# Optimization experiments

Hardware: AMD Instinct MI355X
Metric: run time of the kernel (lower is better)

Reference implementation:

```python
import jax, jax.numpy as jnp
import numpy as np

D_MODEL = 1024
N_HEAD = 16
HEAD_DIM = D_MODEL // N_HEAD


def setup_inputs() -> dict:
    key = jax.random.key(0)
    ks = jax.random.split(key, 11)
    B, L = 1, 2048
    s = 1.0 / np.sqrt(D_MODEL)
    return {
        "q": jax.random.normal(ks[0], (B, L, D_MODEL), jnp.float32),
        "k": jax.random.normal(ks[1], (B, L, D_MODEL), jnp.float32),
        "v": jax.random.normal(ks[2], (B, L, D_MODEL), jnp.float32),
        "w_q": jax.random.normal(ks[3], (D_MODEL, D_MODEL), jnp.float32) * s,
        "b_q": jax.random.normal(ks[4], (D_MODEL,), jnp.float32) * s,
        "w_k": jax.random.normal(ks[5], (D_MODEL, D_MODEL), jnp.float32) * s,
        "b_k": jax.random.normal(ks[6], (D_MODEL,), jnp.float32) * s,
        "w_v": jax.random.normal(ks[7], (D_MODEL, D_MODEL), jnp.float32) * s,
        "b_v": jax.random.normal(ks[8], (D_MODEL,), jnp.float32) * s,
        "w_o": jax.random.normal(ks[9], (D_MODEL, D_MODEL), jnp.float32) * s,
        "b_o": jax.random.normal(ks[10], (D_MODEL,), jnp.float32) * s,
    }


def _split_heads(x):
    # [B, L, D] -> [B, H, L, Dh]
    B, L, D = x.shape
    return x.reshape(B, L, N_HEAD, HEAD_DIM).transpose(0, 2, 1, 3)


def reference(q, k, v, w_q, b_q, w_k, b_k, w_v, b_v, w_o, b_o):
    # Linear projections (torch Linear: x @ W.T + b; here weights stored as [D_in, D_out])
    qh = _split_heads(q @ w_q + b_q)
    kh = _split_heads(k @ w_k + b_k)
    vh = _split_heads(v @ w_v + b_v)
    scale = 1.0 / jnp.sqrt(jnp.asarray(HEAD_DIM, qh.dtype))
    # [B, H, Lq, Lk] full score matrix (faithful to naive implementation)
    score = jnp.einsum("bhqd,bhkd->bhqk", qh, kh) * scale
    attn = jax.nn.softmax(score, axis=-1)
    out = jnp.einsum("bhqk,bhkd->bhqd", attn, vh)
    # concat heads: [B, H, L, Dh] -> [B, L, D]
    B, H, L, Dh = out.shape
    out = out.transpose(0, 2, 1, 3).reshape(B, L, H * Dh)
    return out @ w_o + b_o  # dropout p=0.0 -> identity
```

## Files before the change

kernel.cpp:

```cpp
#include <hip/hip_runtime.h>
#include <hip/hip_bf16.h>
#include <stdint.h>
#include <stddef.h>

typedef __bf16 bf16_t;
typedef __bf16 v8bf __attribute__((ext_vector_type(8)));
typedef __bf16 v4bf __attribute__((ext_vector_type(4)));
typedef float  v4f  __attribute__((ext_vector_type(4)));

#define L_SEQ 2048
#define DM    1024
#define NH    16
#define LOG2E 1.44269504088896340736f
#define SCL   (0.125f * LOG2E)

__device__ __forceinline__ void async_cp16(const void* g, void* l) {
  __builtin_amdgcn_global_load_lds(
      (__attribute__((address_space(1))) void*)(g),
      (__attribute__((address_space(3))) void*)(l),
      16, 0, 0);
}

__device__ __forceinline__ v4f mfma16(v8bf a, v8bf b, v4f c) {
  return __builtin_amdgcn_mfma_f32_16x16x32_bf16(a, b, c, 0, 0, 0);
}

#if __has_builtin(__builtin_amdgcn_exp2f)
__device__ __forceinline__ float fast_exp2(float x) { return __builtin_amdgcn_exp2f(x); }
#else
__device__ __forceinline__ float fast_exp2(float x) { return exp2f(x); }
#endif

__global__ void k_prep(
    const float* __restrict__ q, const float* __restrict__ k,
    const float* __restrict__ v,
    const float* __restrict__ w0, const float* __restrict__ w1,
    const float* __restrict__ w2, const float* __restrict__ w3,
    bf16_t* __restrict__ Qb, bf16_t* __restrict__ Kb, bf16_t* __restrict__ Vb,
    bf16_t* __restrict__ o0, bf16_t* __restrict__ o1,
    bf16_t* __restrict__ o2, bf16_t* __restrict__ o3)
{
  const int z = blockIdx.z;
  const int tid = threadIdx.x;
  if (z < 4) {
    const float* in = (z == 0) ? w0 : (z == 1) ? w1 : (z == 2) ? w2 : w3;
    bf16_t*     out = (z == 0) ? o0 : (z == 1) ? o1 : (z == 2) ? o2 : o3;
    __shared__ float t[64 * 65];
    const int r0 = blockIdx.y * 64, c0 = blockIdx.x * 64;
#pragma unroll
    for (int p = 0; p < 16; ++p) {
      const int idx = p * 256 + tid;
      const int r = idx >> 6, c = idx & 63;
      t[r * 65 + c] = in[(size_t)(r0 + r) * DM + c0 + c];
    }
    __syncthreads();
#pragma unroll
    for (int p = 0; p < 16; ++p) {
      const int idx = p * 256 + tid;
      const int c = idx >> 6, r = idx & 63;
      out[(size_t)(c0 + c) * DM + r0 + r] = (bf16_t)t[r * 65 + c];
    }
  } else {
    const float* src = (z == 4) ? q : (z == 5) ? k : v;
    bf16_t*      dst = (z == 4) ? Qb : (z == 5) ? Kb : Vb;
    const int n4 = (L_SEQ * DM) / 4;
    const int base = (blockIdx.y * 16 + blockIdx.x) * 256 + tid;
#pragma unroll
    for (int i = base; i < n4; i += 16 * 16 * 256) {
      v4f x = ((const v4f*)src)[i];
      v4bf y;
      y[0] = (bf16_t)x[0]; y[1] = (bf16_t)x[1];
      y[2] = (bf16_t)x[2]; y[3] = (bf16_t)x[3];
      ((v4bf*)dst)[i] = y;
    }
  }
}

template <typename OutT>
__device__ __forceinline__ void gemm128x64_body(
    const bf16_t* __restrict__ A, const bf16_t* __restrict__ Bt,
    const float* __restrict__ biasN, const float* __restrict__ biasM,
    OutT* __restrict__ C, int M, int N, int K, int bx, int by)
{
  __shared__ __align__(16) bf16_t As[2][128 * 64];
  __shared__ __align__(16) bf16_t Bs[2][64 * 64];
  const int tid  = threadIdx.x;
  const int w    = tid >> 6;
  const int lane = tid & 63;
  const int l16  = lane & 15;
  const int q4   = lane >> 4;
  const int m0   = by * 128, n0 = bx * 64;
  const int wm   = (w >> 1) * 64, wn = (w & 1) * 32;
  const int lr = lane >> 3, lc = lane & 7;

  v4f acc[4][2];
#pragma unroll
  for (int i = 0; i < 4; ++i)
#pragma unroll
    for (int j = 0; j < 2; ++j) {
      v4f z = {0.f, 0.f, 0.f, 0.f};
      acc[i][j] = z;
    }

  auto stage = [&](int k0, int buf) {
#pragma unroll
    for (int c = 0; c < 4; ++c) {
      const int row = 32 * w + 8 * c + lr;
      const int q   = lc ^ (row & 7);
      async_cp16(A + (size_t)(m0 + row) * K + k0 + q * 8,
                 &As[buf][(32 * w + 8 * c) * 64]);
    }
#pragma unroll
    for (int c = 0; c < 2; ++c) {
      const int row = 16 * w + 8 * c + lr;
      const int q   = lc ^ (row & 7);
      async_cp16(Bt + (size_t)(n0 + row) * K + k0 + q * 8,
                 &Bs[buf][(16 * w + 8 * c) * 64]);
    }
  };

  stage(0, 0);
  __syncthreads();

  const int nk = K >> 6;
  for (int kt = 0; kt < nk; ++kt) {
    if (kt + 1 < nk) stage((kt + 1) << 6, (kt + 1) & 1);
    const int buf = kt & 1;
#pragma unroll
    for (int ks = 0; ks < 2; ++ks) {
      v8bf af[4], bf_[2];
#pragma unroll
      for (int mi = 0; mi < 4; ++mi) {
        const int row = wm + mi * 16 + l16;
        const int pc  = (4 * ks + q4) ^ (row & 7);
        af[mi] = *(const v8bf*)(&As[buf][row * 64 + pc * 8]);
      }
#pragma unroll
      for (int ni = 0; ni < 2; ++ni) {
        const int row = wn + ni * 16 + l16;
        const int pc  = (4 * ks + q4) ^ (row & 7);
        bf_[ni] = *(const v8bf*)(&Bs[buf][row * 64 + pc * 8]);
      }
#pragma unroll
      for (int mi = 0; mi < 4; ++mi)
#pragma unroll
        for (int ni = 0; ni < 2; ++ni)
          acc[mi][ni] = mfma16(af[mi], bf_[ni], acc[mi][ni]);
    }
    __syncthreads();
  }

  float bvn[2] = {0.f, 0.f};
  if (biasN) {
#pragma unroll
    for (int ni = 0; ni < 2; ++ni) bvn[ni] = biasN[n0 + wn + ni * 16 + l16];
  }
#pragma unroll
  for (int mi = 0; mi < 4; ++mi) {
#pragma unroll
    for (int r = 0; r < 4; ++r) {
      const int row = m0 + wm + mi * 16 + q4 * 4 + r;
      const float bm = biasM ? biasM[row] : 0.f;
#pragma unroll
      for (int ni = 0; ni < 2; ++ni) {
        const int col = n0 + wn + ni * 16 + l16;
        C[(size_t)row * N + col] = (OutT)(acc[mi][ni][r] + bvn[ni] + bm);
      }
    }
  }
}

__global__ __launch_bounds__(256, 3) void k_gemm_fused(
    const bf16_t* __restrict__ Qb, const bf16_t* __restrict__ Kb,
    const bf16_t* __restrict__ Vb,
    const bf16_t* __restrict__ Wqkt,
    const bf16_t* __restrict__ Wvt,
    const float* __restrict__ bq, const float* __restrict__ bk,
    const float* __restrict__ bv,
    bf16_t* __restrict__ QKo, bf16_t* __restrict__ Vtr)
{
  const int idx = blockIdx.x;
  const bf16_t *A, *Bt;
  const float *bN = nullptr, *bM = nullptr;
  bf16_t* C;
  int M, N, bx, by;
  if (idx < 512) {
    by = idx & 15; bx = idx >> 4;
    A  = (bx < 16) ? Qb : Kb;
    Bt = Wqkt;
    bN = (bx < 16) ? bq : (bk - DM);
    C  = QKo; M = L_SEQ; N = 2 * DM;
  } else {
    const int i2 = idx - 512;
    by = i2 & 7; bx = i2 >> 3;
    A  = Wvt; Bt = Vb; bM = bv;
    C  = Vtr; M = DM; N = L_SEQ;
  }
  gemm128x64_body<bf16_t>(A, Bt, bN, bM, C, M, N, DM, bx, by);
}

__global__ __launch_bounds__(256, 3) void k_gemm_oproj(
    const bf16_t* __restrict__ A, const bf16_t* __restrict__ Bt,
    const float* __restrict__ bias, float* __restrict__ C)
{
  gemm128x64_body<float>(A, Bt, bias, nullptr, C, L_SEQ, DM, DM,
                         blockIdx.x, blockIdx.y);
}

__global__ __launch_bounds__(256, 2) void k_attn(
    const bf16_t* __restrict__ QKp,
    const bf16_t* __restrict__ Vt,
    bf16_t* __restrict__ AO)
{
  constexpr int LD = 2 * DM;
  const int lid = blockIdx.x;
  const int hd  = (lid & 7) + 8 * ((lid >> 3) & 1);
  const int q0  = (lid >> 4) * 64;
  const int tid = threadIdx.x, w = tid >> 6, lane = tid & 63;
  const int l16 = lane & 15, q4 = lane >> 4;
  const int lr8 = lane >> 3, lc8 = lane & 7;

  __shared__ __align__(16) bf16_t Ks[2][64 * 64];
  __shared__ __align__(16) bf16_t Vs[2][64 * 64];
  __shared__ __align__(16) bf16_t QPs[64 * 72];

  const bf16_t* Qp = QKp;
  const bf16_t* Kp = QKp + DM;

  const bf16_t* pK[2];
  const bf16_t* pV[2];
#pragma unroll
  for (int c = 0; c < 2; ++c) {
    const int row = 16 * w + 8 * c + lr8;
    const int q   = lc8 ^ (row & 7);
    pK[c] = Kp + (size_t)row * LD + hd * 64 + q * 8;
    pV[c] = Vt + (size_t)(hd * 64 + row) * L_SEQ + q * 8;
  }
  auto stage_kv = [&](int j0, int buf) {
#pragma unroll
    for (int c = 0; c < 2; ++c) {
      async_cp16(pK[c] + (size_t)j0 * LD, &Ks[buf][(16 * w + 8 * c) * 64]);
      async_cp16(pV[c] + j0,              &Vs[buf][(16 * w + 8 * c) * 64]);
    }
  };

#pragma unroll
  for (int c = 0; c < 2; ++c) {
    const int row = 16 * w + 8 * c + lr8;
    const int q   = lc8 ^ (row & 7);
    async_cp16(Qp + (size_t)(q0 + row) * LD + hd * 64 + q * 8,
               &QPs[(16 * w + 8 * c) * 64]);
  }
  stage_kv(0, 0);
  __syncthreads();

  const int prow = 16 * w + l16;
  v8bf bq[2];
#pragma unroll
  for (int ks = 0; ks < 2; ++ks) {
    const int pc = (4 * ks + q4) ^ (prow & 7);
    bq[ks] = *(const v8bf*)(&QPs[prow * 64 + pc * 8]);
  }
  __syncthreads();

  float l_run = 0.f;
  v4f od[4];
#pragma unroll
  for (int d = 0; d < 4; ++d) { v4f z = {0.f, 0.f, 0.f, 0.f}; od[d] = z; }

  for (int jt = 0; jt < L_SEQ / 64; ++jt) {
    if (jt + 1 < L_SEQ / 64) stage_kv((jt + 1) * 64, (jt + 1) & 1);
    const int buf = jt & 1;

    v4f st[4];
#pragma unroll
    for (int nf = 0; nf < 4; ++nf) {
      v4f a0 = {0.f, 0.f, 0.f, 0.f};
      const int rowk = nf * 16 + l16;
#pragma unroll
      for (int ks = 0; ks < 2; ++ks) {
        const int pc = (4 * ks + q4) ^ (rowk & 7);
        v8bf ak = *(const v8bf*)(&Ks[buf][rowk * 64 + pc * 8]);
        a0 = mfma16(ak, bq[ks], a0);
      }
      st[nf] = a0;
    }

#pragma unroll
    for (int nf = 0; nf < 4; ++nf) {
      v4bf pb;
#pragma unroll
      for (int r = 0; r < 4; ++r) {
        const float p = fast_exp2(st[nf][r] * SCL);
        l_run += p;
        pb[r] = (bf16_t)p;
      }
      *(v4bf*)(&QPs[prow * 72 + nf * 16 + q4 * 4]) = pb;
    }

#pragma unroll
    for (int ks = 0; ks < 2; ++ks) {
      v8bf bp = *(const v8bf*)(&QPs[prow * 72 + ks * 32 + q4 * 8]);
#pragma unroll
      for (int dd = 0; dd < 4; ++dd) {
        const int rowv = dd * 16 + l16;
        const int pc   = (4 * ks + q4) ^ (rowv & 7);
        v8bf av = *(const v8bf*)(&Vs[buf][rowv * 64 + pc * 8]);
        od[dd] = mfma16(av, bp, od[dd]);
      }
    }
    __syncthreads();
  }

  l_run += __shfl_xor(l_run, 16, 64);
  l_run += __shfl_xor(l_run, 32, 64);
  const float inv = 1.f / l_run;
  const int rowo = q0 + prow;
#pragma unroll
  for (int dd = 0; dd < 4; ++dd) {
    v4bf ob;
#pragma unroll
    for (int r = 0; r < 4; ++r) ob[r] = (bf16_t)(od[dd][r] * inv);
    *(v4bf*)(&AO[(size_t)rowo * DM + hd * 64 + dd * 16 + q4 * 4]) = ob;
  }
}

extern "C" void kernel_launch(void* const* d_in, const int* in_sizes, int n_in,
                              void* d_out, int out_size, void* d_ws, size_t ws_size,
                              hipStream_t stream)
{
  const float* q  = (const float*)d_in[0];
  const float* k  = (const float*)d_in[1];
  const float* v  = (const float*)d_in[2];
  const float* wq = (const float*)d_in[3];
  const float* bq = (const float*)d_in[4];
  const float* wk = (const float*)d_in[5];
  const float* bk = (const float*)d_in[6];
  const float* wv = (const float*)d_in[7];
  const float* bv = (const float*)d_in[8];
  const float* wo = (const float*)d_in[9];
  const float* bo = (const float*)d_in[10];
  float* out = (float*)d_out;

  const size_t SZ = (size_t)L_SEQ * DM;
  bf16_t* ws   = (bf16_t*)d_ws;
  bf16_t* Qb   = ws;
  bf16_t* Kb   = Qb + SZ;
  bf16_t* Vb   = Kb + SZ;
  bf16_t* QK   = Vb + SZ;
  bf16_t* Vtr  = QK + 2 * SZ;
  bf16_t* AO   = Vtr + SZ;
  bf16_t* Wqt  = AO + SZ;
  bf16_t* Wkt  = Wqt + (size_t)DM * DM;
  bf16_t* Wvt  = Wkt + (size_t)DM * DM;
  bf16_t* Wot  = Wvt + (size_t)DM * DM;

  k_prep<<<dim3(16, 16, 7), 256, 0, stream>>>(q, k, v, wq, wk, wv, wo,
                                              Qb, Kb, Vb, Wqt, Wkt, Wvt, Wot);
  k_gemm_fused<<<dim3(768), 256, 0, stream>>>(Qb, Kb, Vb, Wqt, Wvt,
                                              bq, bk, bv, QK, Vtr);
  k_attn<<<dim3(512), 256, 0, stream>>>(QK, Vtr, AO);
  k_gemm_oproj<<<dim3(16, 16), 256, 0, stream>>>(AO, Wot, bo, out);
}
```

Before: 173.3 us.

## Vectorize weight transpose stores, shrink oproj tile, double KV stage size in attention

The weight transpose now writes four bf16 values per store instead of one scalar. The GEMM body is templated on the M tile, and the output projection uses a 64-row tile with a grid twice as large to fill more compute units. The attention kernel now stages two 64-key tiles per barrier, halving the number of syncs, and raises wave priority around the MFMA sections with s_setprio. The larger K/V buffers double the attention kernel's LDS use, which may reduce occupancy.

```diff
diff --git a/kernel.cpp b/kernel.cpp
--- a/kernel.cpp
+++ b/kernel.cpp
@@ -55,10 +55,14 @@
     }
     __syncthreads();
 #pragma unroll
-    for (int p = 0; p < 16; ++p) {
+    for (int p = 0; p < 4; ++p) {
       const int idx = p * 256 + tid;
-      const int c = idx >> 6, r = idx & 63;
-      out[(size_t)(c0 + c) * DM + r0 + r] = (bf16_t)t[r * 65 + c];
+      const int c  = idx >> 4;
+      const int r4 = (idx & 15) * 4;
+      v4bf y;
+#pragma unroll
+      for (int j = 0; j < 4; ++j) y[j] = (bf16_t)t[(r4 + j) * 65 + c];
+      *(v4bf*)(&out[(size_t)(c0 + c) * DM + r0 + r4]) = y;
     }
   } else {
     const float* src = (z == 4) ? q : (z == 5) ? k : v;
@@ -76,26 +80,27 @@
   }
 }
 
-template <typename OutT>
-__device__ __forceinline__ void gemm128x64_body(
+template <int MI, typename OutT>
+__device__ __forceinline__ void gemm_body(
     const bf16_t* __restrict__ A, const bf16_t* __restrict__ Bt,
     const float* __restrict__ biasN, const float* __restrict__ biasM,
     OutT* __restrict__ C, int M, int N, int K, int bx, int by)
 {
-  __shared__ __align__(16) bf16_t As[2][128 * 64];
+  constexpr int BM = MI * 32;
+  __shared__ __align__(16) bf16_t As[2][BM * 64];
   __shared__ __align__(16) bf16_t Bs[2][64 * 64];
   const int tid  = threadIdx.x;
   const int w    = tid >> 6;
   const int lane = tid & 63;
   const int l16  = lane & 15;
   const int q4   = lane >> 4;
-  const int m0   = by * 128, n0 = bx * 64;
-  const int wm   = (w >> 1) * 64, wn = (w & 1) * 32;
+  const int m0   = by * BM, n0 = bx * 64;
+  const int wm   = (w >> 1) * (MI * 16), wn = (w & 1) * 32;
   const int lr = lane >> 3, lc = lane & 7;
 
-  v4f acc[4][2];
-#pragma unroll
-  for (int i = 0; i < 4; ++i)
+  v4f acc[MI][2];
+#pragma unroll
+  for (int i = 0; i < MI; ++i)
 #pragma unroll
     for (int j = 0; j < 2; ++j) {
       v4f z = {0.f, 0.f, 0.f, 0.f};
@@ -104,11 +109,11 @@
 
   auto stage = [&](int k0, int buf) {
 #pragma unroll
-    for (int c = 0; c < 4; ++c) {
-      const int row = 32 * w + 8 * c + lr;
+    for (int c = 0; c < MI; ++c) {
+      const int row = (BM / 4) * w + 8 * c + lr;
       const int q   = lc ^ (row & 7);
       async_cp16(A + (size_t)(m0 + row) * K + k0 + q * 8,
-                 &As[buf][(32 * w + 8 * c) * 64]);
+                 &As[buf][((BM / 4) * w + 8 * c) * 64]);
     }
 #pragma unroll
     for (int c = 0; c < 2; ++c) {
@@ -128,9 +133,9 @@
     const int buf = kt & 1;
 #pragma unroll
     for (int ks = 0; ks < 2; ++ks) {
-      v8bf af[4], bf_[2];
-#pragma unroll
-      for (int mi = 0; mi < 4; ++mi) {
+      v8bf af[MI], bf_[2];
+#pragma unroll
+      for (int mi = 0; mi < MI; ++mi) {
         const int row = wm + mi * 16 + l16;
         const int pc  = (4 * ks + q4) ^ (row & 7);
         af[mi] = *(const v8bf*)(&As[buf][row * 64 + pc * 8]);
@@ -142,7 +147,7 @@
         bf_[ni] = *(const v8bf*)(&Bs[buf][row * 64 + pc * 8]);
       }
 #pragma unroll
-      for (int mi = 0; mi < 4; ++mi)
+      for (int mi = 0; mi < MI; ++mi)
 #pragma unroll
         for (int ni = 0; ni < 2; ++ni)
           acc[mi][ni] = mfma16(af[mi], bf_[ni], acc[mi][ni]);
@@ -156,7 +161,7 @@
     for (int ni = 0; ni < 2; ++ni) bvn[ni] = biasN[n0 + wn + ni * 16 + l16];
   }
 #pragma unroll
-  for (int mi = 0; mi < 4; ++mi) {
+  for (int mi = 0; mi < MI; ++mi) {
 #pragma unroll
     for (int r = 0; r < 4; ++r) {
       const int row = m0 + wm + mi * 16 + q4 * 4 + r;
@@ -196,15 +201,15 @@
     A  = Wvt; Bt = Vb; bM = bv;
     C  = Vtr; M = DM; N = L_SEQ;
   }
-  gemm128x64_body<bf16_t>(A, Bt, bN, bM, C, M, N, DM, bx, by);
-}
-
-__global__ __launch_bounds__(256, 3) void k_gemm_oproj(
+  gemm_body<4, bf16_t>(A, Bt, bN, bM, C, M, N, DM, bx, by);
+}
+
+__global__ __launch_bounds__(256, 2) void k_gemm_oproj(
     const bf16_t* __restrict__ A, const bf16_t* __restrict__ Bt,
     const float* __restrict__ bias, float* __restrict__ C)
 {
-  gemm128x64_body<float>(A, Bt, bias, nullptr, C, L_SEQ, DM, DM,
-                         blockIdx.x, blockIdx.y);
+  gemm_body<2, float>(A, Bt, bias, nullptr, C, L_SEQ, DM, DM,
+                      blockIdx.x, blockIdx.y);
 }
 
 __global__ __launch_bounds__(256, 2) void k_attn(
@@ -220,8 +225,8 @@
   const int l16 = lane & 15, q4 = lane >> 4;
   const int lr8 = lane >> 3, lc8 = lane & 7;
 
-  __shared__ __align__(16) bf16_t Ks[2][64 * 64];
-  __shared__ __align__(16) bf16_t Vs[2][64 * 64];
+  __shared__ __align__(16) bf16_t Ks[2][2][64 * 64];
+  __shared__ __align__(16) bf16_t Vs[2][2][64 * 64];
   __shared__ __align__(16) bf16_t QPs[64 * 72];
 
   const bf16_t* Qp = QKp;
@@ -236,11 +241,16 @@
     pK[c] = Kp + (size_t)row * LD + hd * 64 + q * 8;
     pV[c] = Vt + (size_t)(hd * 64 + row) * L_SEQ + q * 8;
   }
-  auto stage_kv = [&](int j0, int buf) {
-#pragma unroll
-    for (int c = 0; c < 2; ++c) {
-      async_cp16(pK[c] + (size_t)j0 * LD, &Ks[buf][(16 * w + 8 * c) * 64]);
-      async_cp16(pV[c] + j0,              &Vs[buf][(16 * w + 8 * c) * 64]);
+  auto stage_kv2 = [&](int j0, int db) {
+#pragma unroll
+    for (int h = 0; h < 2; ++h) {
+#pragma unroll
+      for (int c = 0; c < 2; ++c) {
+        async_cp16(pK[c] + (size_t)(j0 + 64 * h) * LD,
+                   &Ks[db][h][(16 * w + 8 * c) * 64]);
+        async_cp16(pV[c] + (j0 + 64 * h),
+                   &Vs[db][h][(16 * w + 8 * c) * 64]);
+      }
     }
   };
 
@@ -251,7 +261,7 @@
     async_cp16(Qp + (size_t)(q0 + row) * LD + hd * 64 + q * 8,
                &QPs[(16 * w + 8 * c) * 64]);
   }
-  stage_kv(0, 0);
+  stage_kv2(0, 0);
   __syncthreads();
 
   const int prow = 16 * w + l16;
@@ -268,46 +278,56 @@
 #pragma unroll
   for (int d = 0; d < 4; ++d) { v4f z = {0.f, 0.f, 0.f, 0.f}; od[d] = z; }
 
-  for (int jt = 0; jt < L_SEQ / 64; ++jt) {
-    if (jt + 1 < L_SEQ / 64) stage_kv((jt + 1) * 64, (jt + 1) & 1);
-    const int buf = jt & 1;
-
-    v4f st[4];
-#pragma unroll
-    for (int nf = 0; nf < 4; ++nf) {
-      v4f a0 = {0.f, 0.f, 0.f, 0.f};
-      const int rowk = nf * 16 + l16;
+  for (int rt = 0; rt < L_SEQ / 128; ++rt) {
+    if (rt + 1 < L_SEQ / 128) stage_kv2((rt + 1) * 128, (rt + 1) & 1);
+    const int db = rt & 1;
+
+#pragma unroll
+    for (int h = 0; h < 2; ++h) {
+      const bf16_t* Kt = Ks[db][h];
+      const bf16_t* Vv = Vs[db][h];
+
+      v4f st[4];
+      __builtin_amdgcn_s_setprio(1);
+#pragma unroll
+      for (int nf = 0; nf < 4; ++nf) {
+        v4f a0 = {0.f, 0.f, 0.f, 0.f};
+        const int rowk = nf * 16 + l16;
+#pragma unroll
+        for (int ks = 0; ks < 2; ++ks) {
+          const int pc = (4 * ks + q4) ^ (rowk & 7);
+          v8bf ak = *(const v8bf*)(&Kt[rowk * 64 + pc * 8]);
+          a0 = mfma16(ak, bq[ks], a0);
+        }
+        st[nf] = a0;
+      }
+      __builtin_amdgcn_s_setprio(0);
+
+#pragma unroll
+      for (int nf = 0; nf < 4; ++nf) {
+        v4bf pb;
+#pragma unroll
+        for (int r = 0; r < 4; ++r) {
+          const float p = fast_exp2(st[nf][r] * SCL);
+          l_run += p;
+          pb[r] = (bf16_t)p;
+        }
+        *(v4bf*)(&QPs[prow * 72 + nf * 16 + q4 * 4]) = pb;
+      }
+
+      __builtin_amdgcn_s_setprio(1);
 #pragma unroll
       for (int ks = 0; ks < 2; ++ks) {
-        const int pc = (4 * ks + q4) ^ (rowk & 7);
-        v8bf ak = *(const v8bf*)(&Ks[buf][rowk * 64 + pc * 8]);
-        a0 = mfma16(ak, bq[ks], a0);
-      }
-      st[nf] = a0;
-    }
-
-#pragma unroll
-    for (int nf = 0; nf < 4; ++nf) {
-      v4bf pb;
-#pragma unroll
-      for (int r = 0; r < 4; ++r) {
-        const float p = fast_exp2(st[nf][r] * SCL);
-        l_run += p;
-        pb[r] = (bf16_t)p;
-      }
-      *(v4bf*)(&QPs[prow * 72 + nf * 16 + q4 * 4]) = pb;
-    }
-
-#pragma unroll
-    for (int ks = 0; ks < 2; ++ks) {
-      v8bf bp = *(const v8bf*)(&QPs[prow * 72 + ks * 32 + q4 * 8]);
-#pragma unroll
-      for (int dd = 0; dd < 4; ++dd) {
-        const int rowv = dd * 16 + l16;
-        const int pc   = (4 * ks + q4) ^ (rowv & 7);
-        v8bf av = *(const v8bf*)(&Vs[buf][rowv * 64 + pc * 8]);
-        od[dd] = mfma16(av, bp, od[dd]);
-      }
+        v8bf bp = *(const v8bf*)(&QPs[prow * 72 + ks * 32 + q4 * 8]);
+#pragma unroll
+        for (int dd = 0; dd < 4; ++dd) {
+          const int rowv = dd * 16 + l16;
+          const int pc   = (4 * ks + q4) ^ (rowv & 7);
+          v8bf av = *(const v8bf*)(&Vv[rowv * 64 + pc * 8]);
+          od[dd] = mfma16(av, bp, od[dd]);
+        }
+      }
+      __builtin_amdgcn_s_setprio(0);
     }
     __syncthreads();
   }
@@ -360,5 +380,5 @@
   k_gemm_fused<<<dim3(768), 256, 0, stream>>>(Qb, Kb, Vb, Wqt, Wvt,
                                               bq, bk, bv, QK, Vtr);
   k_attn<<<dim3(512), 256, 0, stream>>>(QK, Vtr, AO);
-  k_gemm_oproj<<<dim3(16, 16), 256, 0, stream>>>(AO, Wot, bo, out);
-}
+  k_gemm_oproj<<<dim3(16, 32), 256, 0, stream>>>(AO, Wot, bo, out);
+}
```

Result: faster. 168.5 us (-2.8%).
